# Optimization experiments

Hardware: AMD Instinct MI355X
Metric: run time of the kernel (lower is better)

Reference implementation:

```python
import jax, jax.numpy as jnp
import numpy as np

B, T, DKQ, DV, EKQ, EV, H, OUT = 8, 2048, 64, 64, 128, 128, 4, 32
FF = 4 * EV
NEG = -1e30  # additive mask value (safe stand-in for -inf)


def _ln(x, g, b, eps=1e-5):
    m = x.mean(-1, keepdims=True)
    var = ((x - m) ** 2).mean(-1, keepdims=True)
    return (x - m) * jax.lax.rsqrt(var + eps) * g + b


def _attn(q, k, v, mask):
    # q,k,v: [n, T, E] -> heads [n, H, T, dh]; NOTE: no 1/sqrt(d) scaling (faithful to source)
    n, t, _ = q.shape
    q = q.reshape(n, t, H, -1).transpose(0, 2, 1, 3)
    k = k.reshape(n, t, H, -1).transpose(0, 2, 1, 3)
    v = v.reshape(n, t, H, -1).transpose(0, 2, 1, 3)
    w = jnp.einsum('bhqd,bhkd->bhqk', q, k) + mask  # [n,H,T,T]
    a = jax.nn.softmax(w, axis=-1)
    o = jnp.einsum('bhqk,bhkd->bhqd', a, v)
    return o.transpose(0, 2, 1, 3).reshape(n, t, -1)


def setup_inputs() -> dict:
    key = jax.random.key(0)
    ks = jax.random.split(key, 32)
    w = lambda k, s: jax.random.normal(k, s, jnp.float32) * 0.02
    DIN_A = DKQ + DV
    return {
        'kq': jax.random.normal(ks[0], (B, T, DKQ), jnp.float32),
        'v': jax.random.normal(ks[1], (B, T, DV), jnp.float32),
        # Layer A (input_dim = DKQ+DV, embed = EV)
        'A_Wk': w(ks[2], (DIN_A, EV)), 'A_bk': jnp.zeros((EV,), jnp.float32),
        'A_Wq': w(ks[3], (DIN_A, EV)), 'A_bq': jnp.zeros((EV,), jnp.float32),
        'A_Wv': w(ks[4], (DIN_A, EV)), 'A_bv': jnp.zeros((EV,), jnp.float32),
        'A_f1W': w(ks[5], (EV, FF)), 'A_f1b': jnp.zeros((FF,), jnp.float32),
        'A_f2W': w(ks[6], (FF, EV)), 'A_f2b': jnp.zeros((EV,), jnp.float32),
        'A_n1g': jnp.ones((EV,), jnp.float32), 'A_n1b': jnp.zeros((EV,), jnp.float32),
        'A_n2g': jnp.ones((EV,), jnp.float32), 'A_n2b': jnp.zeros((EV,), jnp.float32),
        # Layer B (kq -> EKQ, vA -> EV)
        'B_Wk': w(ks[7], (DKQ, EKQ)), 'B_bk': jnp.zeros((EKQ,), jnp.float32),
        'B_Wq': w(ks[8], (DKQ, EKQ)), 'B_bq': jnp.zeros((EKQ,), jnp.float32),
        'B_Wv': w(ks[9], (EV, EV)), 'B_bv': jnp.zeros((EV,), jnp.float32),
        'B_f1W': w(ks[10], (EV, FF)), 'B_f1b': jnp.zeros((FF,), jnp.float32),
        'B_f2W': w(ks[11], (FF, EV)), 'B_f2b': jnp.zeros((EV,), jnp.float32),
        # Output head
        'out_W': w(ks[12], (EV, OUT)), 'out_b': jnp.zeros((OUT,), jnp.float32),
    }


def reference(kq, v, A_Wk, A_bk, A_Wq, A_bq, A_Wv, A_bv, A_f1W, A_f1b, A_f2W, A_f2b,
              A_n1g, A_n1b, A_n2g, A_n2b, B_Wk, B_bk, B_Wq, B_bq, B_Wv, B_bv,
              B_f1W, B_f1b, B_f2W, B_f2b, out_W, out_b):
    n, t, _ = kq.shape
    i = jnp.arange(t)[:, None]
    j = jnp.arange(t)[None, :]
    mask_a = jnp.where(j <= i, 0.0, NEG).astype(jnp.float32)               # causal (diag=1)
    mask_b = jnp.where((j < i) | ((i == 0) & (j == 0)), 0.0, NEG).astype(jnp.float32)  # strict causal + (0,0) exception

    # ---- Layer A ----
    X = jnp.concatenate([kq, v], axis=-1)
    K = X @ A_Wk + A_bk
    Q = X @ A_Wq + A_bq
    V = X @ A_Wv + A_bv
    attn_out = _attn(Q, K, V, mask_a)
    h1 = _ln(V + attn_out, A_n1g, A_n1b)
    ff = jax.nn.gelu(h1 @ A_f1W + A_f1b, approximate=False) @ A_f2W + A_f2b
    vA = _ln(h1 + ff, A_n2g, A_n2b)

    # ---- Layer B (no residuals / norms: values is overwritten in source) ----
    K2 = kq @ B_Wk + B_bk
    Q2 = kq @ B_Wq + B_bq
    V2 = vA @ B_Wv + B_bv
    attn_out2 = _attn(Q2, K2, V2, mask_b)
    ff2 = jax.nn.gelu(attn_out2 @ B_f1W + B_f1b, approximate=False) @ B_f2W + B_f2b

    return ff2 @ out_W + out_b
```

## Files before the change

kernel.cpp:

```cpp
#include <hip/hip_runtime.h>
#include <hip/hip_bf16.h>

#define TSEQ 2048
#define NBATCH 8
#define NROWS (NBATCH*TSEQ)
#define EMB 128
#define NH 4
#define DH 32
#define OUTD 32
#define APLANE (NROWS*EMB)

typedef short s8v __attribute__((ext_vector_type(8)));
typedef short s4v __attribute__((ext_vector_type(4)));
typedef float f4v __attribute__((ext_vector_type(4)));

__device__ __forceinline__ unsigned short f2bf(float f){
  unsigned int u = __float_as_uint(f);
  unsigned int r = u + 0x7fffu + ((u >> 16) & 1u);
  return (unsigned short)(r >> 16);
}
__device__ __forceinline__ float bf2f(unsigned short u){
  return __uint_as_float(((unsigned int)u) << 16);
}

struct WPack {
  const float* src[10];
  int off[10];
  int ntk[10];
  int rowoff[10];
  int nsh[10];
  int kn[10];
};
__global__ __launch_bounds__(256) void prep(WPack p, short* __restrict__ warena,
                                            const float* __restrict__ kq, const float* __restrict__ v,
                                            unsigned short* __restrict__ X){
  int blk = blockIdx.x;
  if (blk < (NROWS*EMB/256)){
    int idx = blk*256 + threadIdx.x;
    int row = idx >> 7, c = idx & 127;
    float val = (c < 64) ? kq[row*64 + c] : v[row*64 + (c-64)];
    unsigned short hi = f2bf(val);
    X[idx]          = hi;
    X[idx + APLANE] = f2bf(val - bf2f(hi));
    return;
  }
  blk -= (NROWS*EMB/256);
  int m = 0;
  #pragma unroll
  for (int i=0;i<10;i++){
    int nb = p.kn[i] >> 8;
    if (blk < nb){ m = i; break; }
    blk -= nb;
  }
  int idx = blk*256 + threadIdx.x;
  float x = p.src[m][idx];
  int nsh = p.nsh[m];
  int n = idx & ((1<<nsh)-1);
  int k = idx >> nsh;
  int K = p.kn[m] >> nsh;
  unsigned short hi = f2bf(x);
  unsigned short lo = f2bf(x - bf2f(hi));
  short* dh = warena + p.off[m] + (size_t)(p.rowoff[m] + n)*K + k;
  dh[0]        = (short)hi;
  dh[p.ntk[m]] = (short)lo;
}

struct GOuts {
  const float* bias[3];
  float* of[3];
  unsigned short* ob[3];
};
template<int CT>
__global__ __launch_bounds__(256) void gemm2(
    const unsigned short* __restrict__ A, int aplane, int lda, int K, int niter,
    const short* __restrict__ wt, int NTK,
    GOuts og, int NT, int nseg, int act,
    unsigned short* __restrict__ vtb, int vcol0){
  __shared__ short As[2][2][64*40];
  const int tid  = threadIdx.x;
  const int w    = tid >> 6;
  const int lane = tid & 63;
  const int col  = lane & 15;
  const int quad = lane >> 4;
  const int row0 = blockIdx.x * 64;
  const int cb   = blockIdx.y*(64*CT) + w*(16*CT) + col;
  const bool two = (aplane != 0);

  f4v acc[4][CT];
  #pragma unroll
  for (int i=0;i<4;i++)
    #pragma unroll
    for (int j=0;j<CT;j++) acc[i][j] = (f4v){0.f,0.f,0.f,0.f};

  const int ar = tid >> 2, ac = (tid & 3)*8;
  const unsigned short* abase = A + (size_t)(row0 + ar)*lda;

  s8v pah, pal;
  pah = *(const s8v*)(abase + ac);
  if (two) pal = *(const s8v*)(abase + aplane + ac);

  const short* wbase[CT];
  #pragma unroll
  for (int ct=0;ct<CT;ct++) wbase[ct] = wt + (size_t)(cb + ct*16)*K + quad*8;

  for (int i=0;i<niter;i++){
    const int buf = i & 1;
    *(s8v*)&As[buf][0][ar*40 + ac] = pah;
    if (two) *(s8v*)&As[buf][1][ar*40 + ac] = pal;
    __syncthreads();
    if (i+1 < niter){
      const int kcol = (i+1)*32 + ac;
      pah = *(const s8v*)(abase + kcol);
      if (two) pal = *(const s8v*)(abase + aplane + kcol);
    }
    s8v bh[CT], bl[CT];
    #pragma unroll
    for (int ct=0;ct<CT;ct++){
      bh[ct] = *(const s8v*)(wbase[ct] + i*32);
      bl[ct] = *(const s8v*)(wbase[ct] + i*32 + NTK);
    }
    #pragma unroll
    for (int rt=0;rt<4;rt++){
      s8v ah = *(const s8v*)&As[buf][0][(rt*16 + col)*40 + quad*8];
      #pragma unroll
      for (int ct=0;ct<CT;ct++)
        acc[rt][ct] = __builtin_amdgcn_mfma_f32_16x16x32_bf16(ah, bh[ct], acc[rt][ct], 0, 0, 0);
      if (two){
        s8v al = *(const s8v*)&As[buf][1][(rt*16 + col)*40 + quad*8];
        #pragma unroll
        for (int ct=0;ct<CT;ct++)
          acc[rt][ct] = __builtin_amdgcn_mfma_f32_16x16x32_bf16(al, bh[ct], acc[rt][ct], 0, 0, 0);
      }
      #pragma unroll
      for (int ct=0;ct<CT;ct++)
        acc[rt][ct] = __builtin_amdgcn_mfma_f32_16x16x32_bf16(ah, bl[ct], acc[rt][ct], 0, 0, 0);
    }
  }

  const int NB = 64*CT;
  const int cb0 = (int)blockIdx.y * NB;
  const bool dotr = (vtb != nullptr) && (cb0 >= vcol0) && (cb0 < vcol0 + 128);
  short* Lt = &As[0][0][0];
  if (dotr) __syncthreads();

  #pragma unroll
  for (int ct=0;ct<CT;ct++){
    const int cg = cb + ct*16;
    int seg, lcol, ldc;
    if (nseg > 1){ seg = cg >> 7; lcol = cg & 127; ldc = 128; }
    else         { seg = 0; lcol = cg; ldc = NT; }
    const float bv = og.bias[seg][lcol];
    float* of = og.of[seg];
    unsigned short* ob = og.ob[seg];
    #pragma unroll
    for (int rt=0;rt<4;rt++){
      s4v pk;
      #pragma unroll
      for (int r=0;r<4;r++){
        const int row = row0 + rt*16 + quad*4 + r;
        float val = acc[rt][ct][r] + bv;
        if (act == 1) val = 0.5f*val*(1.f + erff(val*0.70710678118654752440f));
        if (ob)      ob[(size_t)row*ldc + lcol] = f2bf(val);
        else if (of) of[(size_t)row*ldc + lcol] = val;
        if (dotr) pk[r] = (short)f2bf(val);
      }
      if (dotr)
        *(s4v*)&Lt[(w*(16*CT) + ct*16 + col)*72 + rt*16 + quad*4] = pk;
    }
  }
  if (dotr){
    __syncthreads();
    const int b = row0 >> 11, t0 = row0 & 2047;
    #pragma unroll
    for (int it=0; it<2*CT; it++){
      const int cl = it*32 + (tid>>3);
      const int t8 = (tid&7)*8;
      s8v o = *(const s8v*)&Lt[cl*72 + t8];
      const int cr = cb0 + cl - vcol0;
      *(s8v*)(vtb + ((size_t)((b*4 + (cr>>5))*32 + (cr&31)))*2048 + t0 + t8) = o;
    }
  }
}

#define KT_STRIDE 40
#define VT_STRIDE 72
#define PW_STRIDE 72
__global__ __launch_bounds__(128) void flash3(const unsigned short* __restrict__ Qb,
                                              const unsigned short* __restrict__ Kb,
                                              const unsigned short* __restrict__ Vtb,
                                              float* __restrict__ O0, float* __restrict__ O1,
                                              float* __restrict__ L0, float* __restrict__ L1,
                                              int mode){
  __shared__ short Kt[64*KT_STRIDE];
  __shared__ short Vt[32*VT_STRIDE];
  __shared__ short Pw[2][16*PW_STRIDE];
  const int tid  = threadIdx.x;
  const int w    = tid >> 6;
  const int lane = tid & 63;
  const int col  = lane & 15;
  const int quad = lane >> 4;
  const int bh = blockIdx.y;
  const int b = bh >> 2, h = bh & 3;
  const int par = blockIdx.z;
  float* Op = par ? O1 : O0;
  float* Lp = par ? L1 : L0;
  const int kr = tid >> 1, kc16 = (tid & 1)*16;
  const int vd = tid >> 2, vk16 = (tid & 3)*16;

  for (int pass = 0; pass < 2; pass++){
    const int t = pass ? blockIdx.x : (63 - blockIdx.x);
    const int qbase = t*32 + w*16;
    const int jtmax = t >> 1;

    s8v qf = *(const s8v*)(Qb + (size_t)(b*TSEQ + qbase + col)*EMB + h*DH + quad*8);
    f4v o0 = {0.f,0.f,0.f,0.f}, o1 = {0.f,0.f,0.f,0.f};
    float lr[4] = {0.f,0.f,0.f,0.f};

    if (par <= jtmax){
      s8v ka, kb2, va, vb;
      {
        const unsigned short* kp = Kb + (size_t)(b*TSEQ + par*64 + kr)*EMB + h*DH + kc16;
        ka = *(const s8v*)kp; kb2 = *(const s8v*)(kp + 8);
        const unsigned short* vp = Vtb + ((size_t)bh*32 + vd)*TSEQ + par*64 + vk16;
        va = *(const s8v*)vp; vb = *(const s8v*)(vp + 8);
      }
      for (int jt = par; jt <= jtmax; jt += 2){
        __syncthreads();
        *(s8v*)&Kt[kr*KT_STRIDE + kc16]     = ka;
        *(s8v*)&Kt[kr*KT_STRIDE + kc16 + 8] = kb2;
        *(s8v*)&Vt[vd*VT_STRIDE + vk16]     = va;
        *(s8v*)&Vt[vd*VT_STRIDE + vk16 + 8] = vb;
        __syncthreads();
        if (jt + 2 <= jtmax){
          const unsigned short* kp = Kb + (size_t)(b*TSEQ + (jt+2)*64 + kr)*EMB + h*DH + kc16;
          ka = *(const s8v*)kp; kb2 = *(const s8v*)(kp + 8);
          const unsigned short* vp = Vtb + ((size_t)bh*32 + vd)*TSEQ + (jt+2)*64 + vk16;
          va = *(const s8v*)vp; vb = *(const s8v*)(vp + 8);
        }
        f4v s[4];
        #pragma unroll
        for (int t4=0;t4<4;t4++){
          s8v kf = *(const s8v*)&Kt[(t4*16 + col)*KT_STRIDE + quad*8];
          f4v z = {0.f,0.f,0.f,0.f};
          s[t4] = __builtin_amdgcn_mfma_f32_16x16x32_bf16(qf, kf, z, 0, 0, 0);
        }
        if (jt == jtmax){
          const int j0 = jt*64;
          #pragma unroll
          for (int t4=0;t4<4;t4++){
            const int jg = j0 + t4*16 + col;
            #pragma unroll
            for (int r=0;r<4;r++){
              const int qg = qbase + quad*4 + r;
              const bool ok = (mode==0) ? (jg <= qg) : ((jg < qg) || (qg==0 && jg==0));
              s[t4][r] = ok ? s[t4][r] : -1e30f;
            }
          }
        }
        #pragma unroll
        for (int t4=0;t4<4;t4++){
          #pragma unroll
          for (int r=0;r<4;r++){
            float pv = __expf(s[t4][r]);
            s[t4][r] = pv;
            lr[r] += pv;
            Pw[w][(quad*4+r)*PW_STRIDE + t4*16 + col] = (short)f2bf(pv);
          }
        }
        #pragma unroll
        for (int kk=0;kk<2;kk++){
          s8v pf  = *(const s8v*)&Pw[w][col*PW_STRIDE + kk*32 + quad*8];
          s8v vf0 = *(const s8v*)&Vt[(col)*VT_STRIDE    + kk*32 + quad*8];
          s8v vf1 = *(const s8v*)&Vt[(16+col)*VT_STRIDE + kk*32 + quad*8];
          o0 = __builtin_amdgcn_mfma_f32_16x16x32_bf16(pf, vf0, o0, 0, 0, 0);
          o1 = __builtin_amdgcn_mfma_f32_16x16x32_bf16(pf, vf1, o1, 0, 0, 0);
        }
      }
    }
    float* obase = Op + (size_t)(b*TSEQ + qbase)*EMB + h*DH;
    #pragma unroll
    for (int r=0;r<4;r++){
      float l = lr[r];
      l += __shfl_xor(l,1); l += __shfl_xor(l,2);
      l += __shfl_xor(l,4); l += __shfl_xor(l,8);
      obase[(size_t)(quad*4+r)*EMB + col]      = o0[r];
      obase[(size_t)(quad*4+r)*EMB + 16 + col] = o1[r];
      if (col == 0) Lp[(size_t)(b*TSEQ + qbase + quad*4 + r)*NH + h] = l;
    }
  }
}

__global__ __launch_bounds__(256) void combine_ln(const float* __restrict__ O0, const float* __restrict__ O1,
                                                  const float* __restrict__ L0, const float* __restrict__ L1,
                                                  const float* __restrict__ Vf,
                                                  const float* __restrict__ g, const float* __restrict__ bt,
                                                  unsigned short* __restrict__ outp){
  const int row = blockIdx.x*4 + (threadIdx.x >> 6);
  const int tid = threadIdx.x & 63;
  const size_t base = (size_t)row*EMB;
  const int h0 = tid >> 5, h1i = 2 + (tid >> 5);
  const float la = L0[(size_t)row*NH + h0] + L1[(size_t)row*NH + h0];
  const float lb = L0[(size_t)row*NH + h1i] + L1[(size_t)row*NH + h1i];
  float x0 = Vf[base+tid]    + (O0[base+tid]    + O1[base+tid])    / la;
  float x1 = Vf[base+tid+64] + (O0[base+tid+64] + O1[base+tid+64]) / lb;
  float s  = x0 + x1;
  float s2 = x0*x0 + x1*x1;
  #pragma unroll
  for (int off=1; off<64; off<<=1){
    s  += __shfl_xor(s,  off);
    s2 += __shfl_xor(s2, off);
  }
  float mean = s * (1.f/128.f);
  float var  = s2 * (1.f/128.f) - mean*mean;
  float rstd = rsqrtf(var + 1e-5f);
  float y0 = (x0-mean)*rstd*g[tid]    + bt[tid];
  float y1 = (x1-mean)*rstd*g[tid+64] + bt[tid+64];
  unsigned short h0b = f2bf(y0), h1b = f2bf(y1);
  outp[base+tid]             = h0b;
  outp[base+tid+64]          = h1b;
  outp[base+tid+APLANE]      = f2bf(y0 - bf2f(h0b));
  outp[base+tid+64+APLANE]   = f2bf(y1 - bf2f(h1b));
}

__global__ __launch_bounds__(256) void ln2(const unsigned short* __restrict__ Xp, const float* __restrict__ R,
                                           const float* __restrict__ g, const float* __restrict__ bt,
                                           unsigned short* __restrict__ outp){
  const int row = blockIdx.x*4 + (threadIdx.x >> 6);
  const int tid = threadIdx.x & 63;
  const size_t base = (size_t)row*EMB;
  float x0 = bf2f(Xp[base+tid])    + bf2f(Xp[base+tid+APLANE])    + R[base+tid];
  float x1 = bf2f(Xp[base+tid+64]) + bf2f(Xp[base+tid+64+APLANE]) + R[base+tid+64];
  float s  = x0 + x1;
  float s2 = x0*x0 + x1*x1;
  #pragma unroll
  for (int off=1; off<64; off<<=1){
    s  += __shfl_xor(s,  off);
    s2 += __shfl_xor(s2, off);
  }
  float mean = s * (1.f/128.f);
  float var  = s2 * (1.f/128.f) - mean*mean;
  float rstd = rsqrtf(var + 1e-5f);
  float y0 = (x0-mean)*rstd*g[tid]    + bt[tid];
  float y1 = (x1-mean)*rstd*g[tid+64] + bt[tid+64];
  unsigned short h0b = f2bf(y0), h1b = f2bf(y1);
  outp[base+tid]             = h0b;
  outp[base+tid+64]          = h1b;
  outp[base+tid+APLANE]      = f2bf(y0 - bf2f(h0b));
  outp[base+tid+64+APLANE]   = f2bf(y1 - bf2f(h1b));
}

__global__ __launch_bounds__(256) void combine_b(const float* __restrict__ O0, const float* __restrict__ O1,
                                                 const float* __restrict__ L0, const float* __restrict__ L1,
                                                 unsigned short* __restrict__ outp){
  const int idx = blockIdx.x*256 + threadIdx.x;
  const int row = idx >> 7, c = idx & 127, h = c >> 5;
  const float l = L0[(size_t)row*NH + h] + L1[(size_t)row*NH + h];
  const float v = (O0[idx] + O1[idx]) / l;
  unsigned short hb = f2bf(v);
  outp[idx]          = hb;
  outp[idx + APLANE] = f2bf(v - bf2f(hb));
}

__global__ __launch_bounds__(256) void out_proj(const float* __restrict__ A,
                                                const float* __restrict__ W, const float* __restrict__ bb,
                                                float* __restrict__ out){
  __shared__ float As[8*128];
  __shared__ float Ws2[128*32];
  const int tid = threadIdx.x;
  const int row0 = blockIdx.x * 8;
  for (int idx = tid; idx < 8*128; idx += 256) As[idx] = A[(size_t)row0*128 + idx];
  for (int idx = tid; idx < 128*32; idx += 256) Ws2[idx] = W[idx];
  __syncthreads();
  const int r = tid >> 5, c = tid & 31;
  float acc = bb[c];
  #pragma unroll 8
  for (int k=0;k<128;k++) acc = fmaf(As[r*128 + k], Ws2[k*32 + c], acc);
  out[(size_t)(row0 + r)*OUTD + c] = acc;
}

extern "C" void kernel_launch(void* const* d_in, const int* in_sizes, int n_in,
                              void* d_out, int out_size, void* d_ws, size_t ws_size,
                              hipStream_t stream) {
  const float* kq    = (const float*)d_in[0];
  const float* v     = (const float*)d_in[1];
  const float* A_Wk  = (const float*)d_in[2];  const float* A_bk  = (const float*)d_in[3];
  const float* A_Wq  = (const float*)d_in[4];  const float* A_bq  = (const float*)d_in[5];
  const float* A_Wv  = (const float*)d_in[6];  const float* A_bv  = (const float*)d_in[7];
  const float* A_f1W = (const float*)d_in[8];  const float* A_f1b = (const float*)d_in[9];
  const float* A_f2W = (const float*)d_in[10]; const float* A_f2b = (const float*)d_in[11];
  const float* A_n1g = (const float*)d_in[12]; const float* A_n1b = (const float*)d_in[13];
  const float* A_n2g = (const float*)d_in[14]; const float* A_n2b = (const float*)d_in[15];
  const float* B_Wk  = (const float*)d_in[16]; const float* B_bk  = (const float*)d_in[17];
  const float* B_Wq  = (const float*)d_in[18]; const float* B_bq  = (const float*)d_in[19];
  const float* B_Wv  = (const float*)d_in[20]; const float* B_bv  = (const float*)d_in[21];
  const float* B_f1W = (const float*)d_in[22]; const float* B_f1b = (const float*)d_in[23];
  const float* B_f2W = (const float*)d_in[24]; const float* B_f2b = (const float*)d_in[25];
  const float* out_W = (const float*)d_in[26]; const float* out_b = (const float*)d_in[27];
  float* out = (float*)d_out;
  (void)in_sizes; (void)n_in; (void)out_size; (void)ws_size;

  char* ws = (char*)d_ws;
  const size_t MB = 1024*1024;
  short* warena = (short*)ws;
  unsigned short* Xs  = (unsigned short*)(ws + 2*MB);
  unsigned short* Qbf = (unsigned short*)(ws + 10*MB);
  unsigned short* Kbf = (unsigned short*)(ws + 14*MB);
  unsigned short* Vtb = (unsigned short*)(ws + 18*MB);
  float* Vf  = (float*)(ws + 22*MB);
  float* O0  = (float*)(ws + 30*MB);
  float* O1  = (float*)(ws + 38*MB);
  float* L0  = (float*)(ws + 46*MB);
  float* L1  = (float*)(ws + 47*MB);
  unsigned short* h1p = (unsigned short*)(ws + 48*MB);
  unsigned short* mid = (unsigned short*)(ws + 56*MB);
  float* ffo = (float*)(ws + 72*MB);
  unsigned short* vAp = (unsigned short*)(ws + 80*MB);

  WPack p;
  const float* srcs[10] = {A_Wq,A_Wk,A_Wv,A_f1W,A_f2W,B_Wq,B_Wk,B_Wv,B_f1W,B_f2W};
  int kn[10]     = {16384,16384,16384,65536,65536,8192,8192,16384,65536,65536};
  int nsh[10]    = {7,7,7,9,7,7,7,7,9,7};
  int off[10]    = {0,0,0,98304,229376,360448,360448,393216,425984,557056};
  int ntk[10]    = {49152,49152,49152,65536,65536,16384,16384,16384,65536,65536};
  int rowoff[10] = {0,128,256,0,0,0,128,0,0,0};
  int nblk = 0;
  for (int i=0;i<10;i++){
    p.src[i]=srcs[i]; p.kn[i]=kn[i]; p.nsh[i]=nsh[i];
    p.off[i]=off[i]; p.ntk[i]=ntk[i]; p.rowoff[i]=rowoff[i];
    nblk += kn[i] >> 8;
  }
  prep<<<(NROWS*EMB/256) + nblk, 256, 0, stream>>>(p, warena, kq, v, Xs);

  GOuts oQKVA = {{A_bq,A_bk,A_bv},{nullptr,nullptr,Vf},{Qbf,Kbf,nullptr}};
  GOuts oF1A  = {{A_f1b,nullptr,nullptr},{nullptr,nullptr,nullptr},{mid,nullptr,nullptr}};
  GOuts oF2A  = {{A_f2b,nullptr,nullptr},{ffo,nullptr,nullptr},{nullptr,nullptr,nullptr}};
  GOuts oQKB  = {{B_bq,B_bk,nullptr},{nullptr,nullptr,nullptr},{Qbf,Kbf,nullptr}};
  GOuts oVB   = {{B_bv,nullptr,nullptr},{nullptr,nullptr,nullptr},{nullptr,nullptr,nullptr}};
  GOuts oF1B  = {{B_f1b,nullptr,nullptr},{nullptr,nullptr,nullptr},{mid,nullptr,nullptr}};
  GOuts oF2B  = {{B_f2b,nullptr,nullptr},{ffo,nullptr,nullptr},{nullptr,nullptr,nullptr}};

  gemm2<2><<<dim3(256,3), 256, 0, stream>>>(Xs, APLANE, 128, 128, 4, warena + 0,      49152, oQKVA, 384, 3, 0, Vtb, 256);
  flash3<<<dim3(32,32,2), 128, 0, stream>>>(Qbf, Kbf, Vtb, O0, O1, L0, L1, 0);
  combine_ln<<<NROWS/4, 256, 0, stream>>>(O0, O1, L0, L1, Vf, A_n1g, A_n1b, h1p);
  gemm2<2><<<dim3(256,4), 256, 0, stream>>>(h1p, APLANE, 128, 128, 4, warena + 98304, 65536, oF1A, 512, 1, 1, nullptr, 0);
  gemm2<1><<<dim3(256,2), 256, 0, stream>>>(mid, 0,      512, 512, 16, warena + 229376, 65536, oF2A, 128, 1, 0, nullptr, 0);
  ln2<<<NROWS/4, 256, 0, stream>>>(h1p, ffo, A_n2g, A_n2b, vAp);

  gemm2<2><<<dim3(256,2), 256, 0, stream>>>(Xs, APLANE, 128, 64, 2,  warena + 360448, 16384, oQKB, 256, 2, 0, nullptr, 0);
  gemm2<1><<<dim3(256,2), 256, 0, stream>>>(vAp, APLANE, 128, 128, 4, warena + 393216, 16384, oVB, 128, 1, 0, Vtb, 0);
  flash3<<<dim3(32,32,2), 128, 0, stream>>>(Qbf, Kbf, Vtb, O0, O1, L0, L1, 1);
  combine_b<<<NROWS*128/256, 256, 0, stream>>>(O0, O1, L0, L1, h1p);
  gemm2<2><<<dim3(256,4), 256, 0, stream>>>(h1p, APLANE, 128, 128, 4, warena + 425984, 65536, oF1B, 512, 1, 1, nullptr, 0);
  gemm2<1><<<dim3(256,2), 256, 0, stream>>>(mid, 0,      512, 512, 16, warena + 557056, 65536, oF2B, 128, 1, 0, nullptr, 0);

  out_proj<<<NROWS/8, 256, 0, stream>>>(ffo, out_W, out_b, out);
}
```

Before: 314.5 us.

## Drop split-K attention partials; normalize in flash kernel and fold log2e into Q

The flash attention kernel no longer splits the key range across two z-blocks with separate O/L partial buffers. Each block now walks all key tiles, normalizes by the row sum itself and writes the final output, bf16 hi/lo pairs in mode 1. That removes the combine_b kernel and the partial-buffer traffic, and simplifies combine_ln. Q is also pre-scaled by log2(e) in the GEMM epilogue so the softmax can use a native exp2 instruction instead of __expf. The trade is half as many flash blocks (1024 instead of 2048) and longer serial loops per block, which may reduce parallelism on the causal workload.

```diff
diff --git a/kernel.cpp b/kernel.cpp
--- a/kernel.cpp
+++ b/kernel.cpp
@@ -9,6 +9,7 @@
 #define DH 32
 #define OUTD 32
 #define APLANE (NROWS*EMB)
+#define LOG2E 1.44269504088896340736f
 
 typedef short s8v __attribute__((ext_vector_type(8)));
 typedef short s4v __attribute__((ext_vector_type(4)));
@@ -21,6 +22,13 @@
 }
 __device__ __forceinline__ float bf2f(unsigned short u){
   return __uint_as_float(((unsigned int)u) << 16);
+}
+__device__ __forceinline__ float exp2fast(float x){
+#if __has_builtin(__builtin_amdgcn_exp2f)
+  return __builtin_amdgcn_exp2f(x);
+#else
+  return __expf(x * 0.6931471805599453f);
+#endif
 }
 
 struct WPack {
@@ -69,6 +77,7 @@
   const float* bias[3];
   float* of[3];
   unsigned short* ob[3];
+  float scl[3];
 };
 template<int CT>
 __global__ __launch_bounds__(256) void gemm2(
@@ -150,6 +159,7 @@
     if (nseg > 1){ seg = cg >> 7; lcol = cg & 127; ldc = 128; }
     else         { seg = 0; lcol = cg; ldc = NT; }
     const float bv = og.bias[seg][lcol];
+    const float sc = og.scl[seg];
     float* of = og.of[seg];
     unsigned short* ob = og.ob[seg];
     #pragma unroll
@@ -160,6 +170,7 @@
         const int row = row0 + rt*16 + quad*4 + r;
         float val = acc[rt][ct][r] + bv;
         if (act == 1) val = 0.5f*val*(1.f + erff(val*0.70710678118654752440f));
+        val *= sc;
         if (ob)      ob[(size_t)row*ldc + lcol] = f2bf(val);
         else if (of) of[(size_t)row*ldc + lcol] = val;
         if (dotr) pk[r] = (short)f2bf(val);
@@ -188,8 +199,8 @@
 __global__ __launch_bounds__(128) void flash3(const unsigned short* __restrict__ Qb,
                                               const unsigned short* __restrict__ Kb,
                                               const unsigned short* __restrict__ Vtb,
-                                              float* __restrict__ O0, float* __restrict__ O1,
-                                              float* __restrict__ L0, float* __restrict__ L1,
+                                              float* __restrict__ Of,
+                                              unsigned short* __restrict__ Ob,
                                               int mode){
   __shared__ short Kt[64*KT_STRIDE];
   __shared__ short Vt[32*VT_STRIDE];
@@ -201,9 +212,6 @@
   const int quad = lane >> 4;
   const int bh = blockIdx.y;
   const int b = bh >> 2, h = bh & 3;
-  const int par = blockIdx.z;
-  float* Op = par ? O1 : O0;
-  float* Lp = par ? L1 : L0;
   const int kr = tid >> 1, kc16 = (tid & 1)*16;
   const int vd = tid >> 2, vk16 = (tid & 3)*16;
 
@@ -216,93 +224,105 @@
     f4v o0 = {0.f,0.f,0.f,0.f}, o1 = {0.f,0.f,0.f,0.f};
     float lr[4] = {0.f,0.f,0.f,0.f};
 
-    if (par <= jtmax){
-      s8v ka, kb2, va, vb;
-      {
-        const unsigned short* kp = Kb + (size_t)(b*TSEQ + par*64 + kr)*EMB + h*DH + kc16;
+    s8v ka, kb2, va, vb;
+    {
+      const unsigned short* kp = Kb + (size_t)(b*TSEQ + kr)*EMB + h*DH + kc16;
+      ka = *(const s8v*)kp; kb2 = *(const s8v*)(kp + 8);
+      const unsigned short* vp = Vtb + ((size_t)bh*32 + vd)*TSEQ + vk16;
+      va = *(const s8v*)vp; vb = *(const s8v*)(vp + 8);
+    }
+    for (int jt = 0; jt <= jtmax; jt++){
+      __syncthreads();
+      *(s8v*)&Kt[kr*KT_STRIDE + kc16]     = ka;
+      *(s8v*)&Kt[kr*KT_STRIDE + kc16 + 8] = kb2;
+      *(s8v*)&Vt[vd*VT_STRIDE + vk16]     = va;
+      *(s8v*)&Vt[vd*VT_STRIDE + vk16 + 8] = vb;
+      __syncthreads();
+      if (jt + 1 <= jtmax){
+        const unsigned short* kp = Kb + (size_t)(b*TSEQ + (jt+1)*64 + kr)*EMB + h*DH + kc16;
         ka = *(const s8v*)kp; kb2 = *(const s8v*)(kp + 8);
-        const unsigned short* vp = Vtb + ((size_t)bh*32 + vd)*TSEQ + par*64 + vk16;
+        const unsigned short* vp = Vtb + ((size_t)bh*32 + vd)*TSEQ + (jt+1)*64 + vk16;
         va = *(const s8v*)vp; vb = *(const s8v*)(vp + 8);
       }
-      for (int jt = par; jt <= jtmax; jt += 2){
-        __syncthreads();
-        *(s8v*)&Kt[kr*KT_STRIDE + kc16]     = ka;
-        *(s8v*)&Kt[kr*KT_STRIDE + kc16 + 8] = kb2;
-        *(s8v*)&Vt[vd*VT_STRIDE + vk16]     = va;
-        *(s8v*)&Vt[vd*VT_STRIDE + vk16 + 8] = vb;
-        __syncthreads();
-        if (jt + 2 <= jtmax){
-          const unsigned short* kp = Kb + (size_t)(b*TSEQ + (jt+2)*64 + kr)*EMB + h*DH + kc16;
-          ka = *(const s8v*)kp; kb2 = *(const s8v*)(kp + 8);
-          const unsigned short* vp = Vtb + ((size_t)bh*32 + vd)*TSEQ + (jt+2)*64 + vk16;
-          va = *(const s8v*)vp; vb = *(const s8v*)(vp + 8);
-        }
-        f4v s[4];
+      f4v s[4];
+      #pragma unroll
+      for (int t4=0;t4<4;t4++){
+        s8v kf = *(const s8v*)&Kt[(t4*16 + col)*KT_STRIDE + quad*8];
+        f4v z = {0.f,0.f,0.f,0.f};
+        s[t4] = __builtin_amdgcn_mfma_f32_16x16x32_bf16(qf, kf, z, 0, 0, 0);
+      }
+      if (jt == jtmax){
+        const int j0 = jt*64;
         #pragma unroll
         for (int t4=0;t4<4;t4++){
-          s8v kf = *(const s8v*)&Kt[(t4*16 + col)*KT_STRIDE + quad*8];
-          f4v z = {0.f,0.f,0.f,0.f};
-          s[t4] = __builtin_amdgcn_mfma_f32_16x16x32_bf16(qf, kf, z, 0, 0, 0);
-        }
-        if (jt == jtmax){
-          const int j0 = jt*64;
+          const int jg = j0 + t4*16 + col;
           #pragma unroll
-          for (int t4=0;t4<4;t4++){
-            const int jg = j0 + t4*16 + col;
-            #pragma unroll
-            for (int r=0;r<4;r++){
-              const int qg = qbase + quad*4 + r;
-              const bool ok = (mode==0) ? (jg <= qg) : ((jg < qg) || (qg==0 && jg==0));
-              s[t4][r] = ok ? s[t4][r] : -1e30f;
-            }
+          for (int r=0;r<4;r++){
+            const int qg = qbase + quad*4 + r;
+            const bool ok = (mode==0) ? (jg <= qg) : ((jg < qg) || (qg==0 && jg==0));
+            s[t4][r] = ok ? s[t4][r] : -1e30f;
           }
         }
+      }
+      #pragma unroll
+      for (int t4=0;t4<4;t4++){
         #pragma unroll
-        for (int t4=0;t4<4;t4++){
-          #pragma unroll
-          for (int r=0;r<4;r++){
-            float pv = __expf(s[t4][r]);
-            s[t4][r] = pv;
-            lr[r] += pv;
-            Pw[w][(quad*4+r)*PW_STRIDE + t4*16 + col] = (short)f2bf(pv);
-          }
+        for (int r=0;r<4;r++){
+          float pv = exp2fast(s[t4][r]);
+          s[t4][r] = pv;
+          lr[r] += pv;
+          Pw[w][(quad*4+r)*PW_STRIDE + t4*16 + col] = (short)f2bf(pv);
         }
-        #pragma unroll
-        for (int kk=0;kk<2;kk++){
-          s8v pf  = *(const s8v*)&Pw[w][col*PW_STRIDE + kk*32 + quad*8];
-          s8v vf0 = *(const s8v*)&Vt[(col)*VT_STRIDE    + kk*32 + quad*8];
-          s8v vf1 = *(const s8v*)&Vt[(16+col)*VT_STRIDE + kk*32 + quad*8];
-          o0 = __builtin_amdgcn_mfma_f32_16x16x32_bf16(pf, vf0, o0, 0, 0, 0);
-          o1 = __builtin_amdgcn_mfma_f32_16x16x32_bf16(pf, vf1, o1, 0, 0, 0);
-        }
-      }
-    }
-    float* obase = Op + (size_t)(b*TSEQ + qbase)*EMB + h*DH;
-    #pragma unroll
-    for (int r=0;r<4;r++){
-      float l = lr[r];
-      l += __shfl_xor(l,1); l += __shfl_xor(l,2);
-      l += __shfl_xor(l,4); l += __shfl_xor(l,8);
-      obase[(size_t)(quad*4+r)*EMB + col]      = o0[r];
-      obase[(size_t)(quad*4+r)*EMB + 16 + col] = o1[r];
-      if (col == 0) Lp[(size_t)(b*TSEQ + qbase + quad*4 + r)*NH + h] = l;
-    }
-  }
-}
-
-__global__ __launch_bounds__(256) void combine_ln(const float* __restrict__ O0, const float* __restrict__ O1,
-                                                  const float* __restrict__ L0, const float* __restrict__ L1,
+      }
+      #pragma unroll
+      for (int kk=0;kk<2;kk++){
+        s8v pf  = *(const s8v*)&Pw[w][col*PW_STRIDE + kk*32 + quad*8];
+        s8v vf0 = *(const s8v*)&Vt[(col)*VT_STRIDE    + kk*32 + quad*8];
+        s8v vf1 = *(const s8v*)&Vt[(16+col)*VT_STRIDE + kk*32 + quad*8];
+        o0 = __builtin_amdgcn_mfma_f32_16x16x32_bf16(pf, vf0, o0, 0, 0, 0);
+        o1 = __builtin_amdgcn_mfma_f32_16x16x32_bf16(pf, vf1, o1, 0, 0, 0);
+      }
+    }
+    if (mode == 0){
+      float* ob = Of + (size_t)(b*TSEQ + qbase)*EMB + h*DH;
+      #pragma unroll
+      for (int r=0;r<4;r++){
+        float l = lr[r];
+        l += __shfl_xor(l,1); l += __shfl_xor(l,2);
+        l += __shfl_xor(l,4); l += __shfl_xor(l,8);
+        float rinv = 1.f/l;
+        ob[(size_t)(quad*4+r)*EMB + col]      = o0[r]*rinv;
+        ob[(size_t)(quad*4+r)*EMB + 16 + col] = o1[r]*rinv;
+      }
+    } else {
+      unsigned short* ob = Ob + (size_t)(b*TSEQ + qbase)*EMB + h*DH;
+      #pragma unroll
+      for (int r=0;r<4;r++){
+        float l = lr[r];
+        l += __shfl_xor(l,1); l += __shfl_xor(l,2);
+        l += __shfl_xor(l,4); l += __shfl_xor(l,8);
+        float rinv = 1.f/l;
+        float v0 = o0[r]*rinv, v1 = o1[r]*rinv;
+        unsigned short h0b = f2bf(v0), h1b = f2bf(v1);
+        const size_t ro = (size_t)(quad*4+r)*EMB;
+        ob[ro + col]               = h0b;
+        ob[ro + 16 + col]          = h1b;
+        ob[ro + col + APLANE]      = f2bf(v0 - bf2f(h0b));
+        ob[ro + 16 + col + APLANE] = f2bf(v1 - bf2f(h1b));
+      }
+    }
+  }
+}
+
+__global__ __launch_bounds__(256) void combine_ln(const float* __restrict__ O,
                                                   const float* __restrict__ Vf,
                                                   const float* __restrict__ g, const float* __restrict__ bt,
                                                   unsigned short* __restrict__ outp){
   const int row = blockIdx.x*4 + (threadIdx.x >> 6);
   const int tid = threadIdx.x & 63;
   const size_t base = (size_t)row*EMB;
-  const int h0 = tid >> 5, h1i = 2 + (tid >> 5);
-  const float la = L0[(size_t)row*NH + h0] + L1[(size_t)row*NH + h0];
-  const float lb = L0[(size_t)row*NH + h1i] + L1[(size_t)row*NH + h1i];
-  float x0 = Vf[base+tid]    + (O0[base+tid]    + O1[base+tid])    / la;
-  float x1 = Vf[base+tid+64] + (O0[base+tid+64] + O1[base+tid+64]) / lb;
+  float x0 = Vf[base+tid]    + O[base+tid];
+  float x1 = Vf[base+tid+64] + O[base+tid+64];
   float s  = x0 + x1;
   float s2 = x0*x0 + x1*x1;
   #pragma unroll
@@ -347,18 +367,6 @@
   outp[base+tid+64]          = h1b;
   outp[base+tid+APLANE]      = f2bf(y0 - bf2f(h0b));
   outp[base+tid+64+APLANE]   = f2bf(y1 - bf2f(h1b));
-}
-
-__global__ __launch_bounds__(256) void combine_b(const float* __restrict__ O0, const float* __restrict__ O1,
-                                                 const float* __restrict__ L0, const float* __restrict__ L1,
-                                                 unsigned short* __restrict__ outp){
-  const int idx = blockIdx.x*256 + threadIdx.x;
-  const int row = idx >> 7, c = idx & 127, h = c >> 5;
-  const float l = L0[(size_t)row*NH + h] + L1[(size_t)row*NH + h];
-  const float v = (O0[idx] + O1[idx]) / l;
-  unsigned short hb = f2bf(v);
-  outp[idx]          = hb;
-  outp[idx + APLANE] = f2bf(v - bf2f(hb));
 }
 
 __global__ __launch_bounds__(256) void out_proj(const float* __restrict__ A,
@@ -408,9 +416,6 @@
   unsigned short* Vtb = (unsigned short*)(ws + 18*MB);
   float* Vf  = (float*)(ws + 22*MB);
   float* O0  = (float*)(ws + 30*MB);
-  float* O1  = (float*)(ws + 38*MB);
-  float* L0  = (float*)(ws + 46*MB);
-  float* L1  = (float*)(ws + 47*MB);
   unsigned short* h1p = (unsigned short*)(ws + 48*MB);
   unsigned short* mid = (unsigned short*)(ws + 56*MB);
   float* ffo = (float*)(ws + 72*MB);
@@ -431,25 +436,24 @@
   }
   prep<<<(NROWS*EMB/256) + nblk, 256, 0, stream>>>(p, warena, kq, v, Xs);
 
-  GOuts oQKVA = {{A_bq,A_bk,A_bv},{nullptr,nullptr,Vf},{Qbf,Kbf,nullptr}};
-  GOuts oF1A  = {{A_f1b,nullptr,nullptr},{nullptr,nullptr,nullptr},{mid,nullptr,nullptr}};
-  GOuts oF2A  = {{A_f2b,nullptr,nullptr},{ffo,nullptr,nullptr},{nullptr,nullptr,nullptr}};
-  GOuts oQKB  = {{B_bq,B_bk,nullptr},{nullptr,nullptr,nullptr},{Qbf,Kbf,nullptr}};
-  GOuts oVB   = {{B_bv,nullptr,nullptr},{nullptr,nullptr,nullptr},{nullptr,nullptr,nullptr}};
-  GOuts oF1B  = {{B_f1b,nullptr,nullptr},{nullptr,nullptr,nullptr},{mid,nullptr,nullptr}};
-  GOuts oF2B  = {{B_f2b,nullptr,nullptr},{ffo,nullptr,nullptr},{nullptr,nullptr,nullptr}};
+  GOuts oQKVA = {{A_bq,A_bk,A_bv},{nullptr,nullptr,Vf},{Qbf,Kbf,nullptr},{LOG2E,1.f,1.f}};
+  GOuts oF1A  = {{A_f1b,nullptr,nullptr},{nullptr,nullptr,nullptr},{mid,nullptr,nullptr},{1.f,1.f,1.f}};
+  GOuts oF2A  = {{A_f2b,nullptr,nullptr},{ffo,nullptr,nullptr},{nullptr,nullptr,nullptr},{1.f,1.f,1.f}};
+  GOuts oQKB  = {{B_bq,B_bk,nullptr},{nullptr,nullptr,nullptr},{Qbf,Kbf,nullptr},{LOG2E,1.f,1.f}};
+  GOuts oVB   = {{B_bv,nullptr,nullptr},{nullptr,nullptr,nullptr},{nullptr,nullptr,nullptr},{1.f,1.f,1.f}};
+  GOuts oF1B  = {{B_f1b,nullptr,nullptr},{nullptr,nullptr,nullptr},{mid,nullptr,nullptr},{1.f,1.f,1.f}};
+  GOuts oF2B  = {{B_f2b,nullptr,nullptr},{ffo,nullptr,nullptr},{nullptr,nullptr,nullptr},{1.f,1.f,1.f}};
 
   gemm2<2><<<dim3(256,3), 256, 0, stream>>>(Xs, APLANE, 128, 128, 4, warena + 0,      49152, oQKVA, 384, 3, 0, Vtb, 256);
-  flash3<<<dim3(32,32,2), 128, 0, stream>>>(Qbf, Kbf, Vtb, O0, O1, L0, L1, 0);
-  combine_ln<<<NROWS/4, 256, 0, stream>>>(O0, O1, L0, L1, Vf, A_n1g, A_n1b, h1p);
+  flash3<<<dim3(32,32), 128, 0, stream>>>(Qbf, Kbf, Vtb, O0, nullptr, 0);
+  combine_ln<<<NROWS/4, 256, 0, stream>>>(O0, Vf, A_n1g, A_n1b, h1p);
   gemm2<2><<<dim3(256,4), 256, 0, stream>>>(h1p, APLANE, 128, 128, 4, warena + 98304, 65536, oF1A, 512, 1, 1, nullptr, 0);
   gemm2<1><<<dim3(256,2), 256, 0, stream>>>(mid, 0,      512, 512, 16, warena + 229376, 65536, oF2A, 128, 1, 0, nullptr, 0);
   ln2<<<NROWS/4, 256, 0, stream>>>(h1p, ffo, A_n2g, A_n2b, vAp);
 
   gemm2<2><<<dim3(256,2), 256, 0, stream>>>(Xs, APLANE, 128, 64, 2,  warena + 360448, 16384, oQKB, 256, 2, 0, nullptr, 0);
   gemm2<1><<<dim3(256,2), 256, 0, stream>>>(vAp, APLANE, 128, 128, 4, warena + 393216, 16384, oVB, 128, 1, 0, Vtb, 0);
-  flash3<<<dim3(32,32,2), 128, 0, stream>>>(Qbf, Kbf, Vtb, O0, O1, L0, L1, 1);
-  combine_b<<<NROWS*128/256, 256, 0, stream>>>(O0, O1, L0, L1, h1p);
+  flash3<<<dim3(32,32), 128, 0, stream>>>(Qbf, Kbf, Vtb, nullptr, h1p, 1);
   gemm2<2><<<dim3(256,4), 256, 0, stream>>>(h1p, APLANE, 128, 128, 4, warena + 425984, 65536, oF1B, 512, 1, 1, nullptr, 0);
   gemm2<1><<<dim3(256,2), 256, 0, stream>>>(mid, 0,      512, 512, 16, warena + 557056, 65536, oF2B, 128, 1, 0, nullptr, 0);
 
```

Result: faster. 306.4 us (-2.6%).

## Use 64-row query tiles with 4-wave flash blocks and exp2 via prescaled Q

Applied to the files above, without the earlier changes.

The flash attention kernel moves from 128-thread blocks that process two 32-row query tiles in paired passes to 256-thread blocks that each handle one 64-row query tile, with a rotated tile index to spread the causal work across blocks. Each thread now loads half as much K/V into shared memory per step. Q is pre-multiplied by log2(e) in the projection GEMM epilogue so the softmax can use a native exp2 instead of __expf. The risk is load imbalance, since blocks no longer pair short and long causal rows, and Q is rounded to bf16 after scaling, which slightly changes precision.

```diff
diff --git a/kernel.cpp b/kernel.cpp
--- a/kernel.cpp
+++ b/kernel.cpp
@@ -9,6 +9,7 @@
 #define DH 32
 #define OUTD 32
 #define APLANE (NROWS*EMB)
+#define LOG2E 1.44269504088896340736f
 
 typedef short s8v __attribute__((ext_vector_type(8)));
 typedef short s4v __attribute__((ext_vector_type(4)));
@@ -21,6 +22,13 @@
 }
 __device__ __forceinline__ float bf2f(unsigned short u){
   return __uint_as_float(((unsigned int)u) << 16);
+}
+__device__ __forceinline__ float exp2fast(float x){
+#if __has_builtin(__builtin_amdgcn_exp2f)
+  return __builtin_amdgcn_exp2f(x);
+#else
+  return __expf(x * 0.6931471805599453f);
+#endif
 }
 
 struct WPack {
@@ -69,6 +77,7 @@
   const float* bias[3];
   float* of[3];
   unsigned short* ob[3];
+  float scl[3];
 };
 template<int CT>
 __global__ __launch_bounds__(256) void gemm2(
@@ -150,6 +159,7 @@
     if (nseg > 1){ seg = cg >> 7; lcol = cg & 127; ldc = 128; }
     else         { seg = 0; lcol = cg; ldc = NT; }
     const float bv = og.bias[seg][lcol];
+    const float sc = og.scl[seg];
     float* of = og.of[seg];
     unsigned short* ob = og.ob[seg];
     #pragma unroll
@@ -160,6 +170,7 @@
         const int row = row0 + rt*16 + quad*4 + r;
         float val = acc[rt][ct][r] + bv;
         if (act == 1) val = 0.5f*val*(1.f + erff(val*0.70710678118654752440f));
+        val *= sc;
         if (ob)      ob[(size_t)row*ldc + lcol] = f2bf(val);
         else if (of) of[(size_t)row*ldc + lcol] = val;
         if (dotr) pk[r] = (short)f2bf(val);
@@ -185,7 +196,7 @@
 #define KT_STRIDE 40
 #define VT_STRIDE 72
 #define PW_STRIDE 72
-__global__ __launch_bounds__(128) void flash3(const unsigned short* __restrict__ Qb,
+__global__ __launch_bounds__(256) void flash4(const unsigned short* __restrict__ Qb,
                                               const unsigned short* __restrict__ Kb,
                                               const unsigned short* __restrict__ Vtb,
                                               float* __restrict__ O0, float* __restrict__ O1,
@@ -193,7 +204,7 @@
                                               int mode){
   __shared__ short Kt[64*KT_STRIDE];
   __shared__ short Vt[32*VT_STRIDE];
-  __shared__ short Pw[2][16*PW_STRIDE];
+  __shared__ short Pw[4][16*PW_STRIDE];
   const int tid  = threadIdx.x;
   const int w    = tid >> 6;
   const int lane = tid & 63;
@@ -204,89 +215,79 @@
   const int par = blockIdx.z;
   float* Op = par ? O1 : O0;
   float* Lp = par ? L1 : L0;
-  const int kr = tid >> 1, kc16 = (tid & 1)*16;
-  const int vd = tid >> 2, vk16 = (tid & 3)*16;
-
-  for (int pass = 0; pass < 2; pass++){
-    const int t = pass ? blockIdx.x : (63 - blockIdx.x);
-    const int qbase = t*32 + w*16;
-    const int jtmax = t >> 1;
-
-    s8v qf = *(const s8v*)(Qb + (size_t)(b*TSEQ + qbase + col)*EMB + h*DH + quad*8);
-    f4v o0 = {0.f,0.f,0.f,0.f}, o1 = {0.f,0.f,0.f,0.f};
-    float lr[4] = {0.f,0.f,0.f,0.f};
-
-    if (par <= jtmax){
-      s8v ka, kb2, va, vb;
-      {
-        const unsigned short* kp = Kb + (size_t)(b*TSEQ + par*64 + kr)*EMB + h*DH + kc16;
-        ka = *(const s8v*)kp; kb2 = *(const s8v*)(kp + 8);
-        const unsigned short* vp = Vtb + ((size_t)bh*32 + vd)*TSEQ + par*64 + vk16;
-        va = *(const s8v*)vp; vb = *(const s8v*)(vp + 8);
-      }
-      for (int jt = par; jt <= jtmax; jt += 2){
-        __syncthreads();
-        *(s8v*)&Kt[kr*KT_STRIDE + kc16]     = ka;
-        *(s8v*)&Kt[kr*KT_STRIDE + kc16 + 8] = kb2;
-        *(s8v*)&Vt[vd*VT_STRIDE + vk16]     = va;
-        *(s8v*)&Vt[vd*VT_STRIDE + vk16 + 8] = vb;
-        __syncthreads();
-        if (jt + 2 <= jtmax){
-          const unsigned short* kp = Kb + (size_t)(b*TSEQ + (jt+2)*64 + kr)*EMB + h*DH + kc16;
-          ka = *(const s8v*)kp; kb2 = *(const s8v*)(kp + 8);
-          const unsigned short* vp = Vtb + ((size_t)bh*32 + vd)*TSEQ + (jt+2)*64 + vk16;
-          va = *(const s8v*)vp; vb = *(const s8v*)(vp + 8);
-        }
-        f4v s[4];
+  const int qt = (int)((blockIdx.x + blockIdx.y) & 31);
+  const int qbase = qt*64 + w*16;
+  const int jtmax = qt;
+
+  const int kr = tid >> 2, kc8 = (tid & 3)*8;
+  const int vd = tid >> 3, vk8 = (tid & 7)*8;
+
+  s8v qf = *(const s8v*)(Qb + (size_t)(b*TSEQ + qbase + col)*EMB + h*DH + quad*8);
+  f4v o0 = {0.f,0.f,0.f,0.f}, o1 = {0.f,0.f,0.f,0.f};
+  float lr[4] = {0.f,0.f,0.f,0.f};
+
+  if (par <= jtmax){
+    s8v ka, va;
+    ka = *(const s8v*)(Kb + (size_t)(b*TSEQ + par*64 + kr)*EMB + h*DH + kc8);
+    va = *(const s8v*)(Vtb + ((size_t)bh*32 + vd)*TSEQ + par*64 + vk8);
+    for (int jt = par; jt <= jtmax; jt += 2){
+      __syncthreads();
+      *(s8v*)&Kt[kr*KT_STRIDE + kc8] = ka;
+      *(s8v*)&Vt[vd*VT_STRIDE + vk8] = va;
+      __syncthreads();
+      if (jt + 2 <= jtmax){
+        ka = *(const s8v*)(Kb + (size_t)(b*TSEQ + (jt+2)*64 + kr)*EMB + h*DH + kc8);
+        va = *(const s8v*)(Vtb + ((size_t)bh*32 + vd)*TSEQ + (jt+2)*64 + vk8);
+      }
+      f4v s[4];
+      #pragma unroll
+      for (int t4=0;t4<4;t4++){
+        s8v kf = *(const s8v*)&Kt[(t4*16 + col)*KT_STRIDE + quad*8];
+        f4v z = {0.f,0.f,0.f,0.f};
+        s[t4] = __builtin_amdgcn_mfma_f32_16x16x32_bf16(qf, kf, z, 0, 0, 0);
+      }
+      if (jt == jtmax){
+        const int j0 = jt*64;
         #pragma unroll
         for (int t4=0;t4<4;t4++){
-          s8v kf = *(const s8v*)&Kt[(t4*16 + col)*KT_STRIDE + quad*8];
-          f4v z = {0.f,0.f,0.f,0.f};
-          s[t4] = __builtin_amdgcn_mfma_f32_16x16x32_bf16(qf, kf, z, 0, 0, 0);
-        }
-        if (jt == jtmax){
-          const int j0 = jt*64;
+          const int jg = j0 + t4*16 + col;
           #pragma unroll
-          for (int t4=0;t4<4;t4++){
-            const int jg = j0 + t4*16 + col;
-            #pragma unroll
-            for (int r=0;r<4;r++){
-              const int qg = qbase + quad*4 + r;
-              const bool ok = (mode==0) ? (jg <= qg) : ((jg < qg) || (qg==0 && jg==0));
-              s[t4][r] = ok ? s[t4][r] : -1e30f;
-            }
+          for (int r=0;r<4;r++){
+            const int qg = qbase + quad*4 + r;
+            const bool ok = (mode==0) ? (jg <= qg) : ((jg < qg) || (qg==0 && jg==0));
+            s[t4][r] = ok ? s[t4][r] : -1e30f;
           }
         }
+      }
+      #pragma unroll
+      for (int t4=0;t4<4;t4++){
         #pragma unroll
-        for (int t4=0;t4<4;t4++){
-          #pragma unroll
-          for (int r=0;r<4;r++){
-            float pv = __expf(s[t4][r]);
-            s[t4][r] = pv;
-            lr[r] += pv;
-            Pw[w][(quad*4+r)*PW_STRIDE + t4*16 + col] = (short)f2bf(pv);
-          }
+        for (int r=0;r<4;r++){
+          float pv = exp2fast(s[t4][r]);
+          s[t4][r] = pv;
+          lr[r] += pv;
+          Pw[w][(quad*4+r)*PW_STRIDE + t4*16 + col] = (short)f2bf(pv);
         }
-        #pragma unroll
-        for (int kk=0;kk<2;kk++){
-          s8v pf  = *(const s8v*)&Pw[w][col*PW_STRIDE + kk*32 + quad*8];
-          s8v vf0 = *(const s8v*)&Vt[(col)*VT_STRIDE    + kk*32 + quad*8];
-          s8v vf1 = *(const s8v*)&Vt[(16+col)*VT_STRIDE + kk*32 + quad*8];
-          o0 = __builtin_amdgcn_mfma_f32_16x16x32_bf16(pf, vf0, o0, 0, 0, 0);
-          o1 = __builtin_amdgcn_mfma_f32_16x16x32_bf16(pf, vf1, o1, 0, 0, 0);
-        }
-      }
-    }
-    float* obase = Op + (size_t)(b*TSEQ + qbase)*EMB + h*DH;
-    #pragma unroll
-    for (int r=0;r<4;r++){
-      float l = lr[r];
-      l += __shfl_xor(l,1); l += __shfl_xor(l,2);
-      l += __shfl_xor(l,4); l += __shfl_xor(l,8);
-      obase[(size_t)(quad*4+r)*EMB + col]      = o0[r];
-      obase[(size_t)(quad*4+r)*EMB + 16 + col] = o1[r];
-      if (col == 0) Lp[(size_t)(b*TSEQ + qbase + quad*4 + r)*NH + h] = l;
-    }
+      }
+      #pragma unroll
+      for (int kk=0;kk<2;kk++){
+        s8v pf  = *(const s8v*)&Pw[w][col*PW_STRIDE + kk*32 + quad*8];
+        s8v vf0 = *(const s8v*)&Vt[(col)*VT_STRIDE    + kk*32 + quad*8];
+        s8v vf1 = *(const s8v*)&Vt[(16+col)*VT_STRIDE + kk*32 + quad*8];
+        o0 = __builtin_amdgcn_mfma_f32_16x16x32_bf16(pf, vf0, o0, 0, 0, 0);
+        o1 = __builtin_amdgcn_mfma_f32_16x16x32_bf16(pf, vf1, o1, 0, 0, 0);
+      }
+    }
+  }
+  float* obase = Op + (size_t)(b*TSEQ + qbase)*EMB + h*DH;
+  #pragma unroll
+  for (int r=0;r<4;r++){
+    float l = lr[r];
+    l += __shfl_xor(l,1); l += __shfl_xor(l,2);
+    l += __shfl_xor(l,4); l += __shfl_xor(l,8);
+    obase[(size_t)(quad*4+r)*EMB + col]      = o0[r];
+    obase[(size_t)(quad*4+r)*EMB + 16 + col] = o1[r];
+    if (col == 0) Lp[(size_t)(b*TSEQ + qbase + quad*4 + r)*NH + h] = l;
   }
 }
 
@@ -431,16 +432,16 @@
   }
   prep<<<(NROWS*EMB/256) + nblk, 256, 0, stream>>>(p, warena, kq, v, Xs);
 
-  GOuts oQKVA = {{A_bq,A_bk,A_bv},{nullptr,nullptr,Vf},{Qbf,Kbf,nullptr}};
-  GOuts oF1A  = {{A_f1b,nullptr,nullptr},{nullptr,nullptr,nullptr},{mid,nullptr,nullptr}};
-  GOuts oF2A  = {{A_f2b,nullptr,nullptr},{ffo,nullptr,nullptr},{nullptr,nullptr,nullptr}};
-  GOuts oQKB  = {{B_bq,B_bk,nullptr},{nullptr,nullptr,nullptr},{Qbf,Kbf,nullptr}};
-  GOuts oVB   = {{B_bv,nullptr,nullptr},{nullptr,nullptr,nullptr},{nullptr,nullptr,nullptr}};
-  GOuts oF1B  = {{B_f1b,nullptr,nullptr},{nullptr,nullptr,nullptr},{mid,nullptr,nullptr}};
-  GOuts oF2B  = {{B_f2b,nullptr,nullptr},{ffo,nullptr,nullptr},{nullptr,nullptr,nullptr}};
+  GOuts oQKVA = {{A_bq,A_bk,A_bv},{nullptr,nullptr,Vf},{Qbf,Kbf,nullptr},{LOG2E,1.f,1.f}};
+  GOuts oF1A  = {{A_f1b,nullptr,nullptr},{nullptr,nullptr,nullptr},{mid,nullptr,nullptr},{1.f,1.f,1.f}};
+  GOuts oF2A  = {{A_f2b,nullptr,nullptr},{ffo,nullptr,nullptr},{nullptr,nullptr,nullptr},{1.f,1.f,1.f}};
+  GOuts oQKB  = {{B_bq,B_bk,nullptr},{nullptr,nullptr,nullptr},{Qbf,Kbf,nullptr},{LOG2E,1.f,1.f}};
+  GOuts oVB   = {{B_bv,nullptr,nullptr},{nullptr,nullptr,nullptr},{nullptr,nullptr,nullptr},{1.f,1.f,1.f}};
+  GOuts oF1B  = {{B_f1b,nullptr,nullptr},{nullptr,nullptr,nullptr},{mid,nullptr,nullptr},{1.f,1.f,1.f}};
+  GOuts oF2B  = {{B_f2b,nullptr,nullptr},{ffo,nullptr,nullptr},{nullptr,nullptr,nullptr},{1.f,1.f,1.f}};
 
   gemm2<2><<<dim3(256,3), 256, 0, stream>>>(Xs, APLANE, 128, 128, 4, warena + 0,      49152, oQKVA, 384, 3, 0, Vtb, 256);
-  flash3<<<dim3(32,32,2), 128, 0, stream>>>(Qbf, Kbf, Vtb, O0, O1, L0, L1, 0);
+  flash4<<<dim3(32,32,2), 256, 0, stream>>>(Qbf, Kbf, Vtb, O0, O1, L0, L1, 0);
   combine_ln<<<NROWS/4, 256, 0, stream>>>(O0, O1, L0, L1, Vf, A_n1g, A_n1b, h1p);
   gemm2<2><<<dim3(256,4), 256, 0, stream>>>(h1p, APLANE, 128, 128, 4, warena + 98304, 65536, oF1A, 512, 1, 1, nullptr, 0);
   gemm2<1><<<dim3(256,2), 256, 0, stream>>>(mid, 0,      512, 512, 16, warena + 229376, 65536, oF2A, 128, 1, 0, nullptr, 0);
@@ -448,7 +449,7 @@
 
   gemm2<2><<<dim3(256,2), 256, 0, stream>>>(Xs, APLANE, 128, 64, 2,  warena + 360448, 16384, oQKB, 256, 2, 0, nullptr, 0);
   gemm2<1><<<dim3(256,2), 256, 0, stream>>>(vAp, APLANE, 128, 128, 4, warena + 393216, 16384, oVB, 128, 1, 0, Vtb, 0);
-  flash3<<<dim3(32,32,2), 128, 0, stream>>>(Qbf, Kbf, Vtb, O0, O1, L0, L1, 1);
+  flash4<<<dim3(32,32,2), 256, 0, stream>>>(Qbf, Kbf, Vtb, O0, O1, L0, L1, 1);
   combine_b<<<NROWS*128/256, 256, 0, stream>>>(O0, O1, L0, L1, h1p);
   gemm2<2><<<dim3(256,4), 256, 0, stream>>>(h1p, APLANE, 128, 128, 4, warena + 425984, 65536, oF1B, 512, 1, 1, nullptr, 0);
   gemm2<1><<<dim3(256,2), 256, 0, stream>>>(mid, 0,      512, 512, 16, warena + 557056, 65536, oF2B, 128, 1, 0, nullptr, 0);
```

Measured after the change: 317.1 us. No clear change (+0.8%).
